# Kernel optimization log

Hardware: AMD Instinct MI355X
Metric: run time of the kernel (lower is better)

## Reference

```python
import jax, jax.numpy as jnp
import numpy as np

N = 100_000   # active voxels
CIN = 64
COUT = 64
K = 3
L = 128       # voxel grid extent per axis
C = K // 2    # kernel center


def _offsets():
    # spatial offsets (z, y, x) for all non-center kernel taps, in the same
    # enumeration order as the original module's triple loop
    offs = []
    for dz in range(K):
        for dy in range(K):
            for dx in range(K):
                if (dz, dy, dx) != (C, C, C):
                    offs.append((dz - C, dy - C, dx - C))
    return offs


def _build_neighbor_map(coords):
    # coords: [N,3] int, unique. For each offset build (out_idx, in_idx) pairs
    # where voxel out_idx has an active neighbor in_idx at coords+offset.
    keys = (coords[:, 0].astype(np.int64) * L + coords[:, 1]) * L + coords[:, 2]
    order = np.argsort(keys)
    skeys = keys[order]
    pairs = []
    for (z, y, x) in _offsets():
        nb = coords + np.array([z, y, x], dtype=coords.dtype)
        valid = np.all((nb >= 0) & (nb < L), axis=1)
        nkeys = (nb[:, 0].astype(np.int64) * L + nb[:, 1]) * L + nb[:, 2]
        pos = np.clip(np.searchsorted(skeys, nkeys), 0, N - 1)
        found = valid & (skeys[pos] == nkeys)
        out_idx = np.nonzero(found)[0].astype(np.int32)
        in_idx = order[pos[found]].astype(np.int32)
        pairs.append((out_idx, in_idx))
    P = max(len(o) for o, _ in pairs)
    nei = np.zeros((len(pairs), P, 2), dtype=np.int32)
    sizes = np.zeros(len(pairs), dtype=np.int32)
    for i, (o, j) in enumerate(pairs):
        nei[i, :len(o), 0] = o
        nei[i, :len(o), 1] = j
        sizes[i] = len(o)
    return nei, sizes


def setup_inputs() -> dict:
    rng = np.random.default_rng(0)
    flat = rng.choice(L * L * L, size=N, replace=False)  # unique voxel coords
    coords = np.stack([flat // (L * L), (flat // L) % L, flat % L], axis=1).astype(np.int32)
    nei, sizes = _build_neighbor_map(coords)
    key = jax.random.key(0)
    k1, k2, k3 = jax.random.split(key, 3)
    sp_values = jax.random.normal(k1, (N, CIN), dtype=jnp.float32)
    weight = jax.random.normal(k2, (COUT, K, K, K, CIN), dtype=jnp.float32) * 0.05
    bias = jax.random.normal(k3, (COUT,), dtype=jnp.float32)
    return {"sp_values": sp_values, "weight": weight, "bias": bias,
            "nei_indices": jnp.asarray(nei), "nei_sizes": jnp.asarray(sizes)}


def reference(sp_values, weight, bias, nei_indices, nei_sizes):
    # weight: [Cout,kz,ky,kx,Cin] -> [kz,ky,kx,Cin,Cout] (matches torch permute)
    w = jnp.transpose(weight, (1, 2, 3, 4, 0))
    out = sp_values @ w[C, C, C]                                   # center tap: [N,Cout]
    offs = _offsets()
    w_offs = jnp.stack([w[z + C, y + C, x + C] for (z, y, x) in offs])  # [O,Cin,Cout]
    P = nei_indices.shape[1]
    valid = (jnp.arange(P)[None, :] < nei_sizes[:, None]).astype(sp_values.dtype)  # [O,P]
    gathered = sp_values[nei_indices[:, :, 1]] * valid[:, :, None]  # [O,P,Cin], padded rows zeroed
    contrib = jnp.einsum('opc,ocd->opd', gathered, w_offs)          # [O,P,Cout]
    out = out.at[nei_indices[:, :, 0].reshape(-1)].add(contrib.reshape(-1, out.shape[1]))
    return out + bias
```

## Files before the change

### kernel.cpp

```cpp
#include <hip/hip_runtime.h>


typedef __bf16 bf16x8 __attribute__((ext_vector_type(8)));
typedef float f32x4 __attribute__((ext_vector_type(4)));

__device__ __forceinline__ unsigned short f2bf(float f) {
    union { float f; unsigned int u; } v; v.f = f;
    unsigned int u = v.u;
    return (unsigned short)((u + 0x7FFFu + ((u >> 16) & 1u)) >> 16);
}

__device__ __forceinline__ ushort4 cvt4(float4 v) {
    ushort4 b;
    b.x = f2bf(v.x); b.y = f2bf(v.y); b.z = f2bf(v.z); b.w = f2bf(v.w);
    return b;
}

__global__ __launch_bounds__(256) void sp3d_prep(
    const float* __restrict__ sp, const float* __restrict__ w,
    unsigned short* __restrict__ spb, unsigned short* __restrict__ wb,
    int* __restrict__ tbl, int n_rows)
{
    const long gt = (long)blockIdx.x * 256 + threadIdx.x;
    const long stride = (long)gridDim.x * 256;

    const long ntbl = 26L * n_rows;
    for (long i = gt; i < (ntbl >> 2); i += stride)
        *(int4*)&tbl[i * 4] = make_int4(-1, -1, -1, -1);
    if (gt < (ntbl & 3)) tbl[(ntbl & ~3L) + gt] = -1;

    const long nsp = (long)n_rows * 16;
    for (long i = gt; i < nsp; i += stride) {
        float4 v = *(const float4*)&sp[i * 4];
        *(ushort4*)&spb[i * 4] = cvt4(v);
    }

    for (long i = gt; i < 27 * 512; i += stride) {
        int tap = (int)(i >> 9);
        int rem = (int)(i & 511);
        int fragid = rem >> 6, lane = rem & 63;
        int nt = fragid >> 1, half = fragid & 1, ml = lane & 15, quad = lane >> 4;
        const float* src = w + (nt * 16 + ml) * 1728 + tap * 64 + half * 32 + quad * 8;
        float4 v0 = *(const float4*)src;
        float4 v1 = *(const float4*)(src + 4);
        *(ushort4*)&wb[i * 8]     = cvt4(v0);
        *(ushort4*)&wb[i * 8 + 4] = cvt4(v1);
    }
}

__global__ __launch_bounds__(256) void sp3d_build(
    const int* __restrict__ nei, const int* __restrict__ sizes,
    int* __restrict__ tbl, int n_rows, int P)
{
    const int o = blockIdx.y;
    const int p = blockIdx.x * 256 + threadIdx.x;
    if (p < sizes[o]) {
        int2 pr = *(const int2*)&nei[(o * P + p) * 2];
        tbl[(long)o * n_rows + pr.x] = pr.y;
    }
}

__global__ __launch_bounds__(256) void sp3d_main(
    const unsigned short* __restrict__ spb, const unsigned short* __restrict__ wb,
    const float* __restrict__ bias, const int* __restrict__ tbl,
    float* __restrict__ out, int n_rows)
{
    const int t = threadIdx.x;
    const int wid = t >> 6, lane = t & 63, ml = lane & 15, quad = lane >> 4;
    const int row0 = blockIdx.x * 64;
    const int mrow = row0 + wid * 16 + ml;
    const bool rowok = mrow < n_rows;

    bf16x8 z8;
    #pragma unroll
    for (int j = 0; j < 8; ++j) z8[j] = (__bf16)0.f;

    f32x4 acc[4];
    #pragma unroll
    for (int nt = 0; nt < 4; ++nt) acc[nt] = f32x4{0.f, 0.f, 0.f, 0.f};

    #define GETV(tn) ((tn) == 13 ? (rowok ? mrow : -1) \
                                 : (rowok ? tbl[(long)((tn) - ((tn) > 13 ? 1 : 0)) * n_rows + mrow] : -1))

    int v0 = GETV(0), v1 = GETV(1);
    bf16x8 a0 = z8, a1 = z8, na0 = z8, na1 = z8;
    if (v0 >= 0) {
        const unsigned short* ap = spb + (long)v0 * 64 + quad * 8;
        a0 = *(const bf16x8*)ap; a1 = *(const bf16x8*)(ap + 32);
    }
    if (v1 >= 0) {
        const unsigned short* ap = spb + (long)v1 * 64 + quad * 8;
        na0 = *(const bf16x8*)ap; na1 = *(const bf16x8*)(ap + 32);
    }
    bf16x8 b[8], nb[8];
    if (__any(v0 >= 0)) {
        #pragma unroll
        for (int j = 0; j < 8; ++j) b[j] = *(const bf16x8*)(wb + j * 512 + lane * 8);
    }

    #pragma unroll
    for (int tp = 0; tp < 27; ++tp) {
        int v2 = -1;
        bf16x8 f0 = z8, f1 = z8;
        if (tp + 2 < 27) {
            v2 = GETV(tp + 2);
            if (v2 >= 0) {
                const unsigned short* ap = spb + (long)v2 * 64 + quad * 8;
                f0 = *(const bf16x8*)ap; f1 = *(const bf16x8*)(ap + 32);
            }
        }
        if (tp + 1 < 27 && __any(v1 >= 0)) {
            #pragma unroll
            for (int j = 0; j < 8; ++j)
                nb[j] = *(const bf16x8*)(wb + (tp + 1) * 4096 + j * 512 + lane * 8);
        }
        if (__any(v0 >= 0)) {
            #pragma unroll
            for (int nt = 0; nt < 4; ++nt) {
                acc[nt] = __builtin_amdgcn_mfma_f32_16x16x32_bf16(a0, b[nt * 2 + 0], acc[nt], 0, 0, 0);
                acc[nt] = __builtin_amdgcn_mfma_f32_16x16x32_bf16(a1, b[nt * 2 + 1], acc[nt], 0, 0, 0);
            }
        }
        v0 = v1; a0 = na0; a1 = na1;
        v1 = v2; na0 = f0; na1 = f1;
        #pragma unroll
        for (int j = 0; j < 8; ++j) b[j] = nb[j];
    }
    #undef GETV

    #pragma unroll
    for (int nt = 0; nt < 4; ++nt) {
        int col = nt * 16 + ml;
        float bv = bias[col];
        #pragma unroll
        for (int rg = 0; rg < 4; ++rg) {
            int row = row0 + wid * 16 + quad * 4 + rg;
            if (row < n_rows) out[(long)row * 64 + col] = acc[nt][rg] + bv;
        }
    }
}

extern "C" void kernel_launch(void* const* d_in, const int* in_sizes, int n_in,
                              void* d_out, int out_size, void* d_ws, size_t ws_size,
                              hipStream_t stream) {
    const float* sp    = (const float*)d_in[0];
    const float* w     = (const float*)d_in[1];
    const float* bias  = (const float*)d_in[2];
    const int*   nei   = (const int*)d_in[3];
    const int*   sizes = (const int*)d_in[4];
    float* out = (float*)d_out;

    const int N = in_sizes[0] / 64;
    const int P = in_sizes[3] / (26 * 2);

    char* ws = (char*)d_ws;
    unsigned short* spb = (unsigned short*)ws;
    size_t off = ((size_t)N * 64 * 2 + 255) & ~(size_t)255;
    unsigned short* wb = (unsigned short*)(ws + off);
    off = (off + 27 * 4096 * 2 + 255) & ~(size_t)255;
    int* tbl = (int*)(ws + off);

    sp3d_prep<<<dim3(2048), 256, 0, stream>>>(sp, w, spb, wb, tbl, N);
    sp3d_build<<<dim3((P + 255) / 256, 26), 256, 0, stream>>>(nei, sizes, tbl, N, P);
    sp3d_main<<<dim3((N + 63) / 64), 256, 0, stream>>>(spb, wb, bias, tbl, out, N);
}
```

Before: 142.0 us.

## Process 64 rows per wave to reuse weight fragments, use zero-row for missing neighbors

The main kernel now uses one 64-thread wave per 64-row block. Each wave handles four 16-row groups, so every weight fragment loaded for a tap feeds four groups of MFMAs instead of one. Missing neighbors read an appended all-zero row in the bf16 feature buffer, which replaces the per-tap branches and the manual two-stage software prefetch. This cuts weight-load traffic and divergence, but it drops the wave-uniform skipping of all-empty taps and raises register pressure through 64 accumulator floats and four A fragments per lane.

```diff
diff --git a/kernel.cpp b/kernel.cpp
--- a/kernel.cpp
+++ b/kernel.cpp
@@ -34,6 +34,10 @@
         float4 v = *(const float4*)&sp[i * 4];
         *(ushort4*)&spb[i * 4] = cvt4(v);
     }
+    if (gt < 16) {
+        ushort4 z; z.x = 0; z.y = 0; z.z = 0; z.w = 0;
+        *(ushort4*)&spb[(long)n_rows * 64 + gt * 4] = z;
+    }
 
     for (long i = gt; i < 27 * 512; i += stride) {
         int tap = (int)(i >> 9);
@@ -60,82 +64,88 @@
     }
 }
 
-__global__ __launch_bounds__(256) void sp3d_main(
+__global__ __launch_bounds__(64) void sp3d_main(
     const unsigned short* __restrict__ spb, const unsigned short* __restrict__ wb,
     const float* __restrict__ bias, const int* __restrict__ tbl,
     float* __restrict__ out, int n_rows)
 {
-    const int t = threadIdx.x;
-    const int wid = t >> 6, lane = t & 63, ml = lane & 15, quad = lane >> 4;
+    const int lane = threadIdx.x;
+    const int ml = lane & 15, quad = lane >> 4;
     const int row0 = blockIdx.x * 64;
-    const int mrow = row0 + wid * 16 + ml;
-    const bool rowok = mrow < n_rows;
 
-    bf16x8 z8;
+    f32x4 acc[4][4];
     #pragma unroll
-    for (int j = 0; j < 8; ++j) z8[j] = (__bf16)0.f;
+    for (int g = 0; g < 4; ++g)
+        #pragma unroll
+        for (int nt = 0; nt < 4; ++nt) acc[g][nt] = f32x4{0.f, 0.f, 0.f, 0.f};
 
-    f32x4 acc[4];
-    #pragma unroll
-    for (int nt = 0; nt < 4; ++nt) acc[nt] = f32x4{0.f, 0.f, 0.f, 0.f};
-
-    #define GETV(tn) ((tn) == 13 ? (rowok ? mrow : -1) \
-                                 : (rowok ? tbl[(long)((tn) - ((tn) > 13 ? 1 : 0)) * n_rows + mrow] : -1))
-
-    int v0 = GETV(0), v1 = GETV(1);
-    bf16x8 a0 = z8, a1 = z8, na0 = z8, na1 = z8;
-    if (v0 >= 0) {
-        const unsigned short* ap = spb + (long)v0 * 64 + quad * 8;
-        a0 = *(const bf16x8*)ap; a1 = *(const bf16x8*)(ap + 32);
-    }
-    if (v1 >= 0) {
-        const unsigned short* ap = spb + (long)v1 * 64 + quad * 8;
-        na0 = *(const bf16x8*)ap; na1 = *(const bf16x8*)(ap + 32);
-    }
-    bf16x8 b[8], nb[8];
-    if (__any(v0 >= 0)) {
+    {
+        bf16x8 b[8];
         #pragma unroll
-        for (int j = 0; j < 8; ++j) b[j] = *(const bf16x8*)(wb + j * 512 + lane * 8);
+        for (int j = 0; j < 8; ++j)
+            b[j] = *(const bf16x8*)(wb + 13 * 4096 + j * 512 + lane * 8);
+        #pragma unroll
+        for (int g = 0; g < 4; ++g) {
+            int r = row0 + g * 16 + ml;
+            int rc = (r < n_rows) ? r : n_rows;
+            const unsigned short* ap = spb + (long)rc * 64 + quad * 8;
+            bf16x8 a0 = *(const bf16x8*)ap;
+            bf16x8 a1 = *(const bf16x8*)(ap + 32);
+            #pragma unroll
+            for (int nt = 0; nt < 4; ++nt) {
+                acc[g][nt] = __builtin_amdgcn_mfma_f32_16x16x32_bf16(a0, b[nt * 2 + 0], acc[g][nt], 0, 0, 0);
+                acc[g][nt] = __builtin_amdgcn_mfma_f32_16x16x32_bf16(a1, b[nt * 2 + 1], acc[g][nt], 0, 0, 0);
+            }
+        }
     }
 
     #pragma unroll
-    for (int tp = 0; tp < 27; ++tp) {
-        int v2 = -1;
-        bf16x8 f0 = z8, f1 = z8;
-        if (tp + 2 < 27) {
-            v2 = GETV(tp + 2);
-            if (v2 >= 0) {
-                const unsigned short* ap = spb + (long)v2 * 64 + quad * 8;
-                f0 = *(const bf16x8*)ap; f1 = *(const bf16x8*)(ap + 32);
+    for (int o = 0; o < 26; ++o) {
+        const int tap = o + (o >= 13 ? 1 : 0);
+
+        int v[4];
+        #pragma unroll
+        for (int g = 0; g < 4; ++g) {
+            int r = row0 + g * 16 + ml;
+            int rc = (r < n_rows) ? r : n_rows - 1;
+            v[g] = tbl[(long)o * n_rows + rc];
+        }
+
+        bf16x8 b[8];
+        #pragma unroll
+        for (int j = 0; j < 8; ++j)
+            b[j] = *(const bf16x8*)(wb + tap * 4096 + j * 512 + lane * 8);
+
+        bf16x8 a0[4], a1[4];
+        #pragma unroll
+        for (int g = 0; g < 4; ++g) {
+            int idx = (v[g] >= 0) ? v[g] : n_rows;
+            const unsigned short* ap = spb + (long)idx * 64 + quad * 8;
+            a0[g] = *(const bf16x8*)ap;
+            a1[g] = *(const bf16x8*)(ap + 32);
+        }
+
+        #pragma unroll
+        for (int g = 0; g < 4; ++g) {
+            #pragma unroll
+            for (int nt = 0; nt < 4; ++nt) {
+                acc[g][nt] = __builtin_amdgcn_mfma_f32_16x16x32_bf16(a0[g], b[nt * 2 + 0], acc[g][nt], 0, 0, 0);
+                acc[g][nt] = __builtin_amdgcn_mfma_f32_16x16x32_bf16(a1[g], b[nt * 2 + 1], acc[g][nt], 0, 0, 0);
             }
         }
-        if (tp + 1 < 27 && __any(v1 >= 0)) {
-            #pragma unroll
-            for (int j = 0; j < 8; ++j)
-                nb[j] = *(const bf16x8*)(wb + (tp + 1) * 4096 + j * 512 + lane * 8);
-        }
-        if (__any(v0 >= 0)) {
-            #pragma unroll
-            for (int nt = 0; nt < 4; ++nt) {
-                acc[nt] = __builtin_amdgcn_mfma_f32_16x16x32_bf16(a0, b[nt * 2 + 0], acc[nt], 0, 0, 0);
-                acc[nt] = __builtin_amdgcn_mfma_f32_16x16x32_bf16(a1, b[nt * 2 + 1], acc[nt], 0, 0, 0);
-            }
-        }
-        v0 = v1; a0 = na0; a1 = na1;
-        v1 = v2; na0 = f0; na1 = f1;
-        #pragma unroll
-        for (int j = 0; j < 8; ++j) b[j] = nb[j];
     }
-    #undef GETV
 
     #pragma unroll
     for (int nt = 0; nt < 4; ++nt) {
         int col = nt * 16 + ml;
         float bv = bias[col];
         #pragma unroll
-        for (int rg = 0; rg < 4; ++rg) {
-            int row = row0 + wid * 16 + quad * 4 + rg;
-            if (row < n_rows) out[(long)row * 64 + col] = acc[nt][rg] + bv;
+        for (int g = 0; g < 4; ++g) {
+            #pragma unroll
+            for (int rg = 0; rg < 4; ++rg) {
+                int row = row0 + g * 16 + quad * 4 + rg;
+                if (row < n_rows) out[(long)row * 64 + col] = acc[g][nt][rg] + bv;
+            }
         }
     }
 }
@@ -155,12 +165,12 @@
 
     char* ws = (char*)d_ws;
     unsigned short* spb = (unsigned short*)ws;
-    size_t off = ((size_t)N * 64 * 2 + 255) & ~(size_t)255;
+    size_t off = ((size_t)(N + 1) * 64 * 2 + 255) & ~(size_t)255;
     unsigned short* wb = (unsigned short*)(ws + off);
     off = (off + 27 * 4096 * 2 + 255) & ~(size_t)255;
     int* tbl = (int*)(ws + off);
 
     sp3d_prep<<<dim3(2048), 256, 0, stream>>>(sp, w, spb, wb, tbl, N);
     sp3d_build<<<dim3((P + 255) / 256, 26), 256, 0, stream>>>(nei, sizes, tbl, N, P);
-    sp3d_main<<<dim3((N + 63) / 64), 256, 0, stream>>>(spb, wb, bias, tbl, out, N);
+    sp3d_main<<<dim3((N + 63) / 64), 64, 0, stream>>>(spb, wb, bias, tbl, out, N);
 }
```

Result: slower. 156.8 us (+10.5%).

## Use zero sentinel row, preload tap indices, deepen branchless gather pipeline

Applied to the files above, without the earlier changes.

Appends a zero row to the bf16 feature buffer so missing neighbours index it rather than taking branches. All 26 neighbour indices are loaded up front, and feature gathers are prefetched three taps ahead through a ring buffer. The __any-guarded conditional loads and MFMAs are removed, and sched_group_barrier hints interleave VMEM loads with MFMAs. Launch bounds now request 3 blocks per CU. This trades the skipping of all-empty taps and extra register pressure for more memory-level parallelism and fewer divergent branches.

```diff
diff --git a/kernel.cpp b/kernel.cpp
--- a/kernel.cpp
+++ b/kernel.cpp
@@ -33,6 +33,10 @@
     for (long i = gt; i < nsp; i += stride) {
         float4 v = *(const float4*)&sp[i * 4];
         *(ushort4*)&spb[i * 4] = cvt4(v);
+    }
+    if (gt < 16) {
+        ushort4 z; z.x = 0; z.y = 0; z.z = 0; z.w = 0;
+        *(ushort4*)&spb[(long)n_rows * 64 + gt * 4] = z;
     }
 
     for (long i = gt; i < 27 * 512; i += stride) {
@@ -60,7 +64,7 @@
     }
 }
 
-__global__ __launch_bounds__(256) void sp3d_main(
+__global__ __launch_bounds__(256, 3) void sp3d_main(
     const unsigned short* __restrict__ spb, const unsigned short* __restrict__ wb,
     const float* __restrict__ bias, const int* __restrict__ tbl,
     float* __restrict__ out, int n_rows)
@@ -70,63 +74,93 @@
     const int row0 = blockIdx.x * 64;
     const int mrow = row0 + wid * 16 + ml;
     const bool rowok = mrow < n_rows;
-
-    bf16x8 z8;
-    #pragma unroll
-    for (int j = 0; j < 8; ++j) z8[j] = (__bf16)0.f;
+    const int mclamp = rowok ? mrow : n_rows - 1;
+
+    int idxs[26];
+    #pragma unroll
+    for (int o = 0; o < 26; ++o) idxs[o] = tbl[(long)o * n_rows + mclamp];
+    #pragma unroll
+    for (int o = 0; o < 26; ++o) idxs[o] = (rowok && idxs[o] >= 0) ? idxs[o] : n_rows;
+    const int cidx = rowok ? mrow : n_rows;
+
+    #define TAPIDX(tn) ((tn) == 13 ? cidx : idxs[(tn) - ((tn) > 13 ? 1 : 0)])
 
     f32x4 acc[4];
     #pragma unroll
     for (int nt = 0; nt < 4; ++nt) acc[nt] = f32x4{0.f, 0.f, 0.f, 0.f};
 
-    #define GETV(tn) ((tn) == 13 ? (rowok ? mrow : -1) \
-                                 : (rowok ? tbl[(long)((tn) - ((tn) > 13 ? 1 : 0)) * n_rows + mrow] : -1))
-
-    int v0 = GETV(0), v1 = GETV(1);
-    bf16x8 a0 = z8, a1 = z8, na0 = z8, na1 = z8;
-    if (v0 >= 0) {
-        const unsigned short* ap = spb + (long)v0 * 64 + quad * 8;
-        a0 = *(const bf16x8*)ap; a1 = *(const bf16x8*)(ap + 32);
-    }
-    if (v1 >= 0) {
-        const unsigned short* ap = spb + (long)v1 * 64 + quad * 8;
-        na0 = *(const bf16x8*)ap; na1 = *(const bf16x8*)(ap + 32);
-    }
-    bf16x8 b[8], nb[8];
-    if (__any(v0 >= 0)) {
-        #pragma unroll
-        for (int j = 0; j < 8; ++j) b[j] = *(const bf16x8*)(wb + j * 512 + lane * 8);
-    }
-
-    #pragma unroll
-    for (int tp = 0; tp < 27; ++tp) {
-        int v2 = -1;
-        bf16x8 f0 = z8, f1 = z8;
-        if (tp + 2 < 27) {
-            v2 = GETV(tp + 2);
-            if (v2 >= 0) {
-                const unsigned short* ap = spb + (long)v2 * 64 + quad * 8;
-                f0 = *(const bf16x8*)ap; f1 = *(const bf16x8*)(ap + 32);
-            }
-        }
-        if (tp + 1 < 27 && __any(v1 >= 0)) {
-            #pragma unroll
-            for (int j = 0; j < 8; ++j)
-                nb[j] = *(const bf16x8*)(wb + (tp + 1) * 4096 + j * 512 + lane * 8);
-        }
-        if (__any(v0 >= 0)) {
-            #pragma unroll
-            for (int nt = 0; nt < 4; ++nt) {
-                acc[nt] = __builtin_amdgcn_mfma_f32_16x16x32_bf16(a0, b[nt * 2 + 0], acc[nt], 0, 0, 0);
-                acc[nt] = __builtin_amdgcn_mfma_f32_16x16x32_bf16(a1, b[nt * 2 + 1], acc[nt], 0, 0, 0);
-            }
-        }
-        v0 = v1; a0 = na0; a1 = na1;
-        v1 = v2; na0 = f0; na1 = f1;
+    bf16x8 pa0[3], pa1[3];
+    #pragma unroll
+    for (int s = 0; s < 3; ++s) {
+        const unsigned short* ap = spb + (long)TAPIDX(s) * 64 + quad * 8;
+        pa0[s] = *(const bf16x8*)ap;
+        pa1[s] = *(const bf16x8*)(ap + 32);
+    }
+    bf16x8 b[8];
+    #pragma unroll
+    for (int j = 0; j < 8; ++j)
+        b[j] = *(const bf16x8*)(wb + j * 512 + lane * 8);
+
+    #pragma unroll
+    for (int tp = 0; tp < 24; ++tp) {
+        const bf16x8 ca0 = pa0[tp % 3];
+        const bf16x8 ca1 = pa1[tp % 3];
+
+        {
+            const unsigned short* ap = spb + (long)TAPIDX(tp + 3) * 64 + quad * 8;
+            pa0[tp % 3] = *(const bf16x8*)ap;
+            pa1[tp % 3] = *(const bf16x8*)(ap + 32);
+        }
+        bf16x8 nb[8];
+        #pragma unroll
+        for (int j = 0; j < 8; ++j)
+            nb[j] = *(const bf16x8*)(wb + (tp + 1) * 4096 + j * 512 + lane * 8);
+
+        #pragma unroll
+        for (int nt = 0; nt < 4; ++nt) {
+            acc[nt] = __builtin_amdgcn_mfma_f32_16x16x32_bf16(ca0, b[nt * 2 + 0], acc[nt], 0, 0, 0);
+            acc[nt] = __builtin_amdgcn_mfma_f32_16x16x32_bf16(ca1, b[nt * 2 + 1], acc[nt], 0, 0, 0);
+        }
         #pragma unroll
         for (int j = 0; j < 8; ++j) b[j] = nb[j];
-    }
-    #undef GETV
+
+        __builtin_amdgcn_sched_group_barrier(0x20, 10, 0);
+        __builtin_amdgcn_sched_group_barrier(0x8, 8, 0);
+    }
+
+    #pragma unroll
+    for (int tp = 24; tp < 26; ++tp) {
+        const bf16x8 ca0 = pa0[tp % 3];
+        const bf16x8 ca1 = pa1[tp % 3];
+
+        bf16x8 nb[8];
+        #pragma unroll
+        for (int j = 0; j < 8; ++j)
+            nb[j] = *(const bf16x8*)(wb + (tp + 1) * 4096 + j * 512 + lane * 8);
+
+        #pragma unroll
+        for (int nt = 0; nt < 4; ++nt) {
+            acc[nt] = __builtin_amdgcn_mfma_f32_16x16x32_bf16(ca0, b[nt * 2 + 0], acc[nt], 0, 0, 0);
+            acc[nt] = __builtin_amdgcn_mfma_f32_16x16x32_bf16(ca1, b[nt * 2 + 1], acc[nt], 0, 0, 0);
+        }
+        #pragma unroll
+        for (int j = 0; j < 8; ++j) b[j] = nb[j];
+
+        __builtin_amdgcn_sched_group_barrier(0x20, 8, 0);
+        __builtin_amdgcn_sched_group_barrier(0x8, 8, 0);
+    }
+
+    {
+        const bf16x8 ca0 = pa0[26 % 3];
+        const bf16x8 ca1 = pa1[26 % 3];
+        #pragma unroll
+        for (int nt = 0; nt < 4; ++nt) {
+            acc[nt] = __builtin_amdgcn_mfma_f32_16x16x32_bf16(ca0, b[nt * 2 + 0], acc[nt], 0, 0, 0);
+            acc[nt] = __builtin_amdgcn_mfma_f32_16x16x32_bf16(ca1, b[nt * 2 + 1], acc[nt], 0, 0, 0);
+        }
+        __builtin_amdgcn_sched_group_barrier(0x8, 8, 0);
+    }
+    #undef TAPIDX
 
     #pragma unroll
     for (int nt = 0; nt < 4; ++nt) {
@@ -155,7 +189,7 @@
 
     char* ws = (char*)d_ws;
     unsigned short* spb = (unsigned short*)ws;
-    size_t off = ((size_t)N * 64 * 2 + 255) & ~(size_t)255;
+    size_t off = ((size_t)(N + 1) * 64 * 2 + 255) & ~(size_t)255;
     unsigned short* wb = (unsigned short*)(ws + off);
     off = (off + 27 * 4096 * 2 + 255) & ~(size_t)255;
     int* tbl = (int*)(ws + off);
```

Result: slower. 149.8 us (+5.5%).

## Branchless zero-row sentinel gathers with inline-asm prefetch pipeline in sparse conv

Applied to the files above, without the earlier changes.

Missing neighbors now point to an appended zero row (index n_rows) instead of -1. This removes the per-tap branches and __any checks, so every tap runs MFMA unconditionally. The main kernel preloads all 26 table indices up front and issues weight and feature loads through inline-asm global_load_dwordx4 with immediate offsets. It uses explicit vmcnt waits to keep a 2-3 stage prefetch pipeline and adds a 3-block occupancy hint. The trade-off is that work on absent taps is no longer skipped, and register pressure rises from the 27 precomputed offsets and double-buffered B fragments.

```diff
diff --git a/kernel.cpp b/kernel.cpp
--- a/kernel.cpp
+++ b/kernel.cpp
@@ -3,6 +3,7 @@
 
 typedef __bf16 bf16x8 __attribute__((ext_vector_type(8)));
 typedef float f32x4 __attribute__((ext_vector_type(4)));
+typedef int   i32x4 __attribute__((ext_vector_type(4)));
 
 __device__ __forceinline__ unsigned short f2bf(float f) {
     union { float f; unsigned int u; } v; v.f = f;
@@ -15,6 +16,14 @@
     b.x = f2bf(v.x); b.y = f2bf(v.y); b.z = f2bf(v.z); b.w = f2bf(v.w);
     return b;
 }
+
+__device__ __forceinline__ bf16x8 asbf(i32x4 v) {
+    union { i32x4 i; bf16x8 b; } u; u.i = v; return u.b;
+}
+
+#define GLD(dst, voff, sbase, IMM) \
+    asm volatile("global_load_dwordx4 %0, %1, %2 offset:" IMM \
+                 : "=&v"(dst) : "v"(voff), "s"(sbase))
 
 __global__ __launch_bounds__(256) void sp3d_prep(
     const float* __restrict__ sp, const float* __restrict__ w,
@@ -25,14 +34,19 @@
     const long stride = (long)gridDim.x * 256;
 
     const long ntbl = 26L * n_rows;
+    const int4 fillv = make_int4(n_rows, n_rows, n_rows, n_rows);
     for (long i = gt; i < (ntbl >> 2); i += stride)
-        *(int4*)&tbl[i * 4] = make_int4(-1, -1, -1, -1);
-    if (gt < (ntbl & 3)) tbl[(ntbl & ~3L) + gt] = -1;
+        *(int4*)&tbl[i * 4] = fillv;
+    if (gt < (ntbl & 3)) tbl[(ntbl & ~3L) + gt] = n_rows;
 
     const long nsp = (long)n_rows * 16;
     for (long i = gt; i < nsp; i += stride) {
         float4 v = *(const float4*)&sp[i * 4];
         *(ushort4*)&spb[i * 4] = cvt4(v);
+    }
+    if (gt < 16) {
+        ushort4 z; z.x = 0; z.y = 0; z.z = 0; z.w = 0;
+        *(ushort4*)&spb[(long)n_rows * 64 + gt * 4] = z;
     }
 
     for (long i = gt; i < 27 * 512; i += stride) {
@@ -60,7 +74,7 @@
     }
 }
 
-__global__ __launch_bounds__(256) void sp3d_main(
+__global__ __launch_bounds__(256, 3) void sp3d_main(
     const unsigned short* __restrict__ spb, const unsigned short* __restrict__ wb,
     const float* __restrict__ bias, const int* __restrict__ tbl,
     float* __restrict__ out, int n_rows)
@@ -70,72 +84,96 @@
     const int row0 = blockIdx.x * 64;
     const int mrow = row0 + wid * 16 + ml;
     const bool rowok = mrow < n_rows;
-
-    bf16x8 z8;
-    #pragma unroll
-    for (int j = 0; j < 8; ++j) z8[j] = (__bf16)0.f;
+    const int rc = rowok ? mrow : 0;
+
+    int voffA[27];
+    #pragma unroll
+    for (int o = 0; o < 26; ++o) {
+        int tap = o + (o >= 13 ? 1 : 0);
+        int idx = tbl[(long)o * n_rows + rc];
+        voffA[tap] = ((rowok ? idx : n_rows) << 7) + quad * 16;
+    }
+    voffA[13] = ((rowok ? mrow : n_rows) << 7) + quad * 16;
+
+    float bv[4];
+    #pragma unroll
+    for (int nt = 0; nt < 4; ++nt) bv[nt] = bias[nt * 16 + ml];
 
     f32x4 acc[4];
     #pragma unroll
     for (int nt = 0; nt < 4; ++nt) acc[nt] = f32x4{0.f, 0.f, 0.f, 0.f};
 
-    #define GETV(tn) ((tn) == 13 ? (rowok ? mrow : -1) \
-                                 : (rowok ? tbl[(long)((tn) - ((tn) > 13 ? 1 : 0)) * n_rows + mrow] : -1))
-
-    int v0 = GETV(0), v1 = GETV(1);
-    bf16x8 a0 = z8, a1 = z8, na0 = z8, na1 = z8;
-    if (v0 >= 0) {
-        const unsigned short* ap = spb + (long)v0 * 64 + quad * 8;
-        a0 = *(const bf16x8*)ap; a1 = *(const bf16x8*)(ap + 32);
-    }
-    if (v1 >= 0) {
-        const unsigned short* ap = spb + (long)v1 * 64 + quad * 8;
-        na0 = *(const bf16x8*)ap; na1 = *(const bf16x8*)(ap + 32);
-    }
-    bf16x8 b[8], nb[8];
-    if (__any(v0 >= 0)) {
-        #pragma unroll
-        for (int j = 0; j < 8; ++j) b[j] = *(const bf16x8*)(wb + j * 512 + lane * 8);
-    }
-
-    #pragma unroll
-    for (int tp = 0; tp < 27; ++tp) {
-        int v2 = -1;
-        bf16x8 f0 = z8, f1 = z8;
-        if (tp + 2 < 27) {
-            v2 = GETV(tp + 2);
-            if (v2 >= 0) {
-                const unsigned short* ap = spb + (long)v2 * 64 + quad * 8;
-                f0 = *(const bf16x8*)ap; f1 = *(const bf16x8*)(ap + 32);
-            }
-        }
-        if (tp + 1 < 27 && __any(v1 >= 0)) {
-            #pragma unroll
-            for (int j = 0; j < 8; ++j)
-                nb[j] = *(const bf16x8*)(wb + (tp + 1) * 4096 + j * 512 + lane * 8);
-        }
-        if (__any(v0 >= 0)) {
-            #pragma unroll
-            for (int nt = 0; nt < 4; ++nt) {
-                acc[nt] = __builtin_amdgcn_mfma_f32_16x16x32_bf16(a0, b[nt * 2 + 0], acc[nt], 0, 0, 0);
-                acc[nt] = __builtin_amdgcn_mfma_f32_16x16x32_bf16(a1, b[nt * 2 + 1], acc[nt], 0, 0, 0);
-            }
-        }
-        v0 = v1; a0 = na0; a1 = na1;
-        v1 = v2; na0 = f0; na1 = f1;
-        #pragma unroll
-        for (int j = 0; j < 8; ++j) b[j] = nb[j];
-    }
-    #undef GETV
+    asm volatile("s_waitcnt vmcnt(0) lgkmcnt(0)" ::: "memory");
+    __builtin_amdgcn_sched_barrier(0);
+
+    const int lb = lane * 16;
+    i32x4 B[2][8], A0[3], A1[3];
+
+    {
+        int vb = lb, vb4 = lb + 4096;
+        GLD(B[0][0], vb,  wb, "0");    GLD(B[0][1], vb,  wb, "1024");
+        GLD(B[0][2], vb,  wb, "2048"); GLD(B[0][3], vb,  wb, "3072");
+        GLD(B[0][4], vb4, wb, "0");    GLD(B[0][5], vb4, wb, "1024");
+        GLD(B[0][6], vb4, wb, "2048"); GLD(B[0][7], vb4, wb, "3072");
+        GLD(A0[0], voffA[0], spb, "0"); GLD(A1[0], voffA[0], spb, "64");
+        GLD(A0[1], voffA[1], spb, "0"); GLD(A1[1], voffA[1], spb, "64");
+    }
+
+    #pragma unroll
+    for (int tp = 0; tp < 25; ++tp) {
+        {
+            int vb = (tp + 1) * 8192 + lb, vb4 = vb + 4096;
+            GLD(B[(tp + 1) & 1][0], vb,  wb, "0");    GLD(B[(tp + 1) & 1][1], vb,  wb, "1024");
+            GLD(B[(tp + 1) & 1][2], vb,  wb, "2048"); GLD(B[(tp + 1) & 1][3], vb,  wb, "3072");
+            GLD(B[(tp + 1) & 1][4], vb4, wb, "0");    GLD(B[(tp + 1) & 1][5], vb4, wb, "1024");
+            GLD(B[(tp + 1) & 1][6], vb4, wb, "2048"); GLD(B[(tp + 1) & 1][7], vb4, wb, "3072");
+            GLD(A0[(tp + 2) % 3], voffA[tp + 2], spb, "0");
+            GLD(A1[(tp + 2) % 3], voffA[tp + 2], spb, "64");
+        }
+        asm volatile("s_waitcnt vmcnt(12)");
+        __builtin_amdgcn_sched_barrier(0);
+        const bf16x8 a0 = asbf(A0[tp % 3]), a1 = asbf(A1[tp % 3]);
+        #pragma unroll
+        for (int nt = 0; nt < 4; ++nt) {
+            acc[nt] = __builtin_amdgcn_mfma_f32_16x16x32_bf16(a0, asbf(B[tp & 1][nt * 2 + 0]), acc[nt], 0, 0, 0);
+            acc[nt] = __builtin_amdgcn_mfma_f32_16x16x32_bf16(a1, asbf(B[tp & 1][nt * 2 + 1]), acc[nt], 0, 0, 0);
+        }
+    }
+
+    {
+        int vb = 26 * 8192 + lb, vb4 = vb + 4096;
+        GLD(B[0][0], vb,  wb, "0");    GLD(B[0][1], vb,  wb, "1024");
+        GLD(B[0][2], vb,  wb, "2048"); GLD(B[0][3], vb,  wb, "3072");
+        GLD(B[0][4], vb4, wb, "0");    GLD(B[0][5], vb4, wb, "1024");
+        GLD(B[0][6], vb4, wb, "2048"); GLD(B[0][7], vb4, wb, "3072");
+        asm volatile("s_waitcnt vmcnt(10)");
+        __builtin_amdgcn_sched_barrier(0);
+        const bf16x8 a0 = asbf(A0[25 % 3]), a1 = asbf(A1[25 % 3]);
+        #pragma unroll
+        for (int nt = 0; nt < 4; ++nt) {
+            acc[nt] = __builtin_amdgcn_mfma_f32_16x16x32_bf16(a0, asbf(B[1][nt * 2 + 0]), acc[nt], 0, 0, 0);
+            acc[nt] = __builtin_amdgcn_mfma_f32_16x16x32_bf16(a1, asbf(B[1][nt * 2 + 1]), acc[nt], 0, 0, 0);
+        }
+    }
+
+    {
+        asm volatile("s_waitcnt vmcnt(0)");
+        __builtin_amdgcn_sched_barrier(0);
+        const bf16x8 a0 = asbf(A0[26 % 3]), a1 = asbf(A1[26 % 3]);
+        #pragma unroll
+        for (int nt = 0; nt < 4; ++nt) {
+            acc[nt] = __builtin_amdgcn_mfma_f32_16x16x32_bf16(a0, asbf(B[0][nt * 2 + 0]), acc[nt], 0, 0, 0);
+            acc[nt] = __builtin_amdgcn_mfma_f32_16x16x32_bf16(a1, asbf(B[0][nt * 2 + 1]), acc[nt], 0, 0, 0);
+        }
+    }
 
     #pragma unroll
     for (int nt = 0; nt < 4; ++nt) {
         int col = nt * 16 + ml;
-        float bv = bias[col];
         #pragma unroll
         for (int rg = 0; rg < 4; ++rg) {
             int row = row0 + wid * 16 + quad * 4 + rg;
-            if (row < n_rows) out[(long)row * 64 + col] = acc[nt][rg] + bv;
+            if (row < n_rows) out[(long)row * 64 + col] = acc[nt][rg] + bv[nt];
         }
     }
 }
@@ -155,7 +193,7 @@
 
     char* ws = (char*)d_ws;
     unsigned short* spb = (unsigned short*)ws;
-    size_t off = ((size_t)N * 64 * 2 + 255) & ~(size_t)255;
+    size_t off = ((size_t)(N + 1) * 64 * 2 + 255) & ~(size_t)255;
     unsigned short* wb = (unsigned short*)(ws + off);
     off = (off + 27 * 4096 * 2 + 255) & ~(size_t)255;
     int* tbl = (int*)(ws + off);
```

After: 148.6 us. 4.7% more time.
